# Kernel tuning notes

Hardware: AMD Instinct MI355X
Metric: run time of the kernel (lower is better)

Reference implementation:

```python
import jax, jax.numpy as jnp
import numpy as np

TEMPERATURE = 0.5


def setup_inputs() -> dict:
    key = jax.random.key(0)
    k1, k2 = jax.random.split(key)
    emb = jax.random.normal(k1, (16384, 128), dtype=jnp.float32)
    emb = emb / jnp.linalg.norm(emb, axis=1, keepdims=True)  # L2-normalized, per docstring
    labels = jax.random.randint(k2, (16384,), 0, 64, dtype=jnp.int64)
    return {"embeddings": emb, "partition_labels": labels}


def reference(embeddings, partition_labels):
    n = embeddings.shape[0]
    # [N, N] similarity matrix, scaled by temperature
    sim = jnp.matmul(embeddings, embeddings.T) / TEMPERATURE
    exp_sim = jnp.exp(sim)
    eye = jnp.eye(n, dtype=bool)
    pos_mask = (partition_labels[None, :] == partition_labels[:, None]) & ~eye
    # numerator: sum of exp over positives; denominator: sum over all k != i
    pos_sum = jnp.sum(jnp.where(pos_mask, exp_sim, 0.0), axis=1)
    all_sum = jnp.sum(jnp.where(~eye, exp_sim, 0.0), axis=1)
    valid = jnp.any(pos_mask, axis=1)
    loss_i = -(jnp.log(pos_sum) - jnp.log(all_sum))
    n_valid = jnp.sum(valid)
    total = jnp.sum(jnp.where(valid, loss_i, 0.0))
    return jnp.where(n_valid > 0, total / n_valid, 0.0)
```

## Files before the change

kernel.cpp:

```cpp
#include <hip/hip_runtime.h>

#define N_EMB 16384
#define DIM 128
#define NLAB 64
#define NSPLIT 8
#define NCT (N_EMB / NSPLIT / 128)
#define NT (N_EMB / 128)

typedef __bf16 bf16x8 __attribute__((ext_vector_type(8)));
typedef float f32x4 __attribute__((ext_vector_type(4)));
typedef unsigned short us8 __attribute__((ext_vector_type(8)));
typedef unsigned short us;
typedef unsigned int u32;

#define SCALE 2.8853900817779268f
#define LN2 0.6931471805599453f

__device__ inline float fexp2(float x) {
#if __has_builtin(__builtin_amdgcn_exp2f)
  return __builtin_amdgcn_exp2f(x);
#else
  return exp2f(x);
#endif
}
__device__ inline float flog2(float x) {
#if __has_builtin(__builtin_amdgcn_logf)
  return __builtin_amdgcn_logf(x);
#else
  return log2f(x);
#endif
}

__device__ inline us f2bf(float f) {
  u32 u = __float_as_uint(f);
  u += 0x7fffu + ((u >> 16) & 1u);
  return (us)(u >> 16);
}

__device__ inline void gll16(const us* g, us* l) {
  __builtin_amdgcn_global_load_lds(
      (const __attribute__((address_space(1))) u32*)g,
      (__attribute__((address_space(3))) u32*)l, 16, 0, 0);
}


__global__ void init_k(int* cntg, float* total) {
  if (threadIdx.x < NLAB) cntg[threadIdx.x] = 0;
  if (threadIdx.x == 0) *total = 0.f;
}

__global__ __launch_bounds__(256) void preconv(const float* __restrict__ emb,
                                               const int* __restrict__ labels,
                                               us* __restrict__ eraw,
                                               us* __restrict__ escal,
                                               int* __restrict__ cntg) {
  __shared__ int h[NLAB];
  const int tid = threadIdx.x;
  if (tid < NLAB) h[tid] = 0;
  __syncthreads();
  if (tid < 128) atomicAdd(&h[labels[blockIdx.x * 128 + tid]], 1);
  const size_t base = (size_t)blockIdx.x * 2048;
#pragma unroll
  for (int i = 0; i < 8; ++i) {
    int g = i * 256 + tid;
    int col16 = g & 15;
    int quad = (g >> 4) & 3;
    int ks = (g >> 6) & 3;
    int tc = g >> 8;
    const float* p = emb + ((size_t)blockIdx.x * 128 + tc * 16 + col16) * DIM +
                     ks * 32 + quad * 8;
    float4 a = *reinterpret_cast<const float4*>(p);
    float4 b = *reinterpret_cast<const float4*>(p + 4);
    us8 r, sc;
    r[0] = f2bf(a.x); r[1] = f2bf(a.y); r[2] = f2bf(a.z); r[3] = f2bf(a.w);
    r[4] = f2bf(b.x); r[5] = f2bf(b.y); r[6] = f2bf(b.z); r[7] = f2bf(b.w);
    sc[0] = f2bf(a.x * SCALE); sc[1] = f2bf(a.y * SCALE);
    sc[2] = f2bf(a.z * SCALE); sc[3] = f2bf(a.w * SCALE);
    sc[4] = f2bf(b.x * SCALE); sc[5] = f2bf(b.y * SCALE);
    sc[6] = f2bf(b.z * SCALE); sc[7] = f2bf(b.w * SCALE);
    *reinterpret_cast<us8*>(eraw + (base + g) * 8) = r;
    *reinterpret_cast<us8*>(escal + (base + g) * 8) = sc;
  }
  __syncthreads();
  if (tid < NLAB && h[tid] > 0) atomicAdd(&cntg[tid], h[tid]);
}

__global__ void scan_k(const int* __restrict__ cntg, int* offp, int* cursor) {
  int tid = threadIdx.x;
  int v = cntg[tid];
  int acc = 0;
#pragma unroll
  for (int k = 0; k < NLAB; ++k) {
    int ck = __shfl(v, k, 64);
    if (k < tid) acc += ck;
  }
  offp[tid] = acc;
  cursor[tid] = acc;
  if (tid == NLAB - 1) offp[NLAB] = acc + v;
}

__global__ void scatter_k(const int* __restrict__ labels, int* cursor,
                          int* perm) {
  __shared__ int lh[NLAB];
  __shared__ int base[NLAB];
  int tid = threadIdx.x;
  int i = blockIdx.x * 256 + tid;
  if (tid < NLAB) lh[tid] = 0;
  __syncthreads();
  int l = labels[i];
  int r = atomicAdd(&lh[l], 1);
  __syncthreads();
  if (tid < NLAB && lh[tid] > 0) base[tid] = atomicAdd(&cursor[tid], lh[tid]);
  __syncthreads();
  perm[base[l] + r] = i;
}

__global__ __launch_bounds__(128, 2) void cl_main(
    const us* __restrict__ eraw, const us* __restrict__ escal,
    float* __restrict__ ws_all) {
  __shared__ us lds[128 * DIM];

  const int tid = threadIdx.x;
  const int lane = tid & 63;
  const int w = tid >> 6;
  const int quad = lane >> 4;
  const int col16 = lane & 15;
  const int r0 = blockIdx.x * 128;
  const int cs = blockIdx.y;

  {
    const us* g = escal + (size_t)blockIdx.x * (128 * DIM);
#pragma unroll
    for (int i = 0; i < 16; ++i) {
      int chunk = i * 2 + w;
      gll16(g + chunk * 512 + lane * 8, lds + chunk * 512);
    }
  }
  __syncthreads();

  bf16x8 afrag[4][4];
#pragma unroll
  for (int tr = 0; tr < 4; ++tr)
#pragma unroll
    for (int ks = 0; ks < 4; ++ks)
      afrag[tr][ks] = *reinterpret_cast<const bf16x8*>(
          lds + ((w * 4 + tr) * 4 + ks) * 512 + lane * 8);

  float all_p[16];
#pragma unroll
  for (int t = 0; t < 16; ++t) all_p[t] = 0.f;

  for (int ct = 0; ct < NCT; ++ct) {
    const int ctg = cs * NCT + ct;
    __syncthreads();
    {
      const us* g = eraw + (size_t)ctg * (128 * DIM);
#pragma unroll
      for (int i = 0; i < 16; ++i) {
        int chunk = i * 2 + w;
        gll16(g + chunk * 512 + lane * 8, lds + chunk * 512);
      }
    }
    __syncthreads();

#pragma unroll
    for (int tc = 0; tc < 8; ++tc) {
      bf16x8 bf[4];
#pragma unroll
      for (int ks = 0; ks < 4; ++ks)
        bf[ks] = *reinterpret_cast<const bf16x8*>(lds + (tc * 4 + ks) * 512 +
                                                  lane * 8);
      const int c = ctg * 128 + tc * 16;
#pragma unroll
      for (int tr = 0; tr < 4; ++tr) {
        f32x4 acc = {0.f, 0.f, 0.f, 0.f};
#pragma unroll
        for (int ks = 0; ks < 4; ++ks)
          acc = __builtin_amdgcn_mfma_f32_16x16x32_bf16(afrag[tr][ks], bf[ks],
                                                        acc, 0, 0, 0);
        const bool diag = c == (r0 + w * 64 + tr * 16);
#pragma unroll
        for (int r = 0; r < 4; ++r) {
          float e = fexp2(acc[r]);
          if (diag && (quad * 4 + r) == col16) e = 0.f;
          all_p[tr * 4 + r] += e;
        }
      }
    }
  }

#pragma unroll
  for (int t = 0; t < 16; ++t) {
    float a = all_p[t];
#pragma unroll
    for (int m = 8; m >= 1; m >>= 1) a += __shfl_xor(a, m, 64);
    if (col16 == 0) {
      int row_g = r0 + w * 64 + (t >> 2) * 16 + quad * 4 + (t & 3);
      ws_all[cs * N_EMB + row_g] = a;
    }
  }
}

__global__ __launch_bounds__(256) void pos_loss(
    const us* __restrict__ eraw, const float* __restrict__ ws_all,
    const int* __restrict__ perm, const int* __restrict__ offp,
    const int* __restrict__ cntg, float* __restrict__ total) {
  const int l = blockIdx.x;
  const int c = cntg[l];
  if (c < 2) return;
  const int off = offp[l];
  const int strips = (c + 15) >> 4;
  const int tid = threadIdx.x;
  const int lane = tid & 63;
  const int w = tid >> 6;
  const int col16 = lane & 15;
  const int quad = lane >> 4;

  __shared__ float sred[4][16];

  bf16x8 zerov;
#pragma unroll
  for (int j = 0; j < 8; ++j) zerov[j] = (__bf16)0.f;

  for (int i = blockIdx.y; i < strips; i += gridDim.y) {
    bf16x8 af[4] = {zerov, zerov, zerov, zerov};
    int rowA = i * 16 + col16;
    if (rowA < c) {
      int rg = perm[off + rowA];
      const us* pA = eraw + ((size_t)(rg >> 7) * 2048 +
                             ((rg & 127) >> 4) * 256 + quad * 16 + (rg & 15)) *
                                8;
#pragma unroll
      for (int ks = 0; ks < 4; ++ks)
        af[ks] = *reinterpret_cast<const bf16x8*>(pA + ks * 512);
    }
    float sum[4] = {0.f, 0.f, 0.f, 0.f};
    for (int j = w; j < strips; j += 4) {
      bf16x8 bf[4] = {zerov, zerov, zerov, zerov};
      int rowB = j * 16 + col16;
      if (rowB < c) {
        int rg = perm[off + rowB];
        const us* pB =
            eraw + ((size_t)(rg >> 7) * 2048 + ((rg & 127) >> 4) * 256 +
                    quad * 16 + (rg & 15)) *
                       8;
#pragma unroll
        for (int ks = 0; ks < 4; ++ks)
          bf[ks] = *reinterpret_cast<const bf16x8*>(pB + ks * 512);
      }
      f32x4 acc = {0.f, 0.f, 0.f, 0.f};
#pragma unroll
      for (int ks = 0; ks < 4; ++ks)
        acc = __builtin_amdgcn_mfma_f32_16x16x32_bf16(af[ks], bf[ks], acc, 0,
                                                      0, 0);
      const float gm = (rowB < c) ? 1.f : 0.f;
#pragma unroll
      for (int r = 0; r < 4; ++r) {
        float e = fexp2(acc[r] * SCALE);
        if (i == j && (quad * 4 + r) == col16) e = 0.f;
        sum[r] = fmaf(e, gm, sum[r]);
      }
    }
#pragma unroll
    for (int r = 0; r < 4; ++r) {
      float s = sum[r];
#pragma unroll
      for (int m = 8; m >= 1; m >>= 1) s += __shfl_xor(s, m, 64);
      if (col16 == 0) sred[w][quad * 4 + r] = s;
    }
    __syncthreads();
    if (tid < 16) {
      int row = i * 16 + tid;
      float t = 0.f;
      if (row < c) {
        float p = sred[0][tid] + sred[1][tid] + sred[2][tid] + sred[3][tid];
        int rg = perm[off + row];
        float a = 0.f;
#pragma unroll
        for (int k = 0; k < NSPLIT; ++k) a += ws_all[k * N_EMB + rg];
        t = flog2(a) - flog2(p);
      }
#pragma unroll
      for (int m = 8; m >= 1; m >>= 1) t += __shfl_xor(t, m, 64);
      if (tid == 0) atomicAdd(total, t);
    }
    __syncthreads();
  }
}

__global__ void final_k(const float* __restrict__ total,
                        const int* __restrict__ cntg,
                        float* __restrict__ out) {
  int tid = threadIdx.x;
  int c = (tid < NLAB && cntg[tid] > 1) ? cntg[tid] : 0;
#pragma unroll
  for (int m = 32; m >= 1; m >>= 1) c += __shfl_xor(c, m, 64);
  if (tid == 0) out[0] = (c > 0) ? (*total) * LN2 / (float)c : 0.f;
}

extern "C" void kernel_launch(void* const* d_in, const int* in_sizes, int n_in,
                              void* d_out, int out_size, void* d_ws,
                              size_t ws_size, hipStream_t stream) {
  const float* emb = (const float*)d_in[0];
  const int* labels = (const int*)d_in[1];

  char* w = (char*)d_ws;
  us* eraw = (us*)w;         w += (size_t)N_EMB * DIM * 2;
  us* escal = (us*)w;        w += (size_t)N_EMB * DIM * 2;
  float* ws_all = (float*)w; w += (size_t)NSPLIT * N_EMB * 4;
  int* perm = (int*)w;       w += (size_t)N_EMB * 4;
  int* offp = (int*)w;       w += (NLAB + 1) * 4;
  int* cntg = (int*)w;       w += NLAB * 4;
  int* cursor = (int*)w;     w += NLAB * 4;
  float* total = (float*)w;

  init_k<<<1, 64, 0, stream>>>(cntg, total);
  preconv<<<NT, 256, 0, stream>>>(emb, labels, eraw, escal, cntg);
  scan_k<<<1, 64, 0, stream>>>(cntg, offp, cursor);
  scatter_k<<<N_EMB / 256, 256, 0, stream>>>(labels, cursor, perm);
  cl_main<<<dim3(NT, NSPLIT), 128, 0, stream>>>(eraw, escal, ws_all);
  pos_loss<<<dim3(NLAB, 20), 256, 0, stream>>>(eraw, ws_all, perm, offp, cntg,
                                               total);
  final_k<<<1, 64, 0, stream>>>(total, cntg, (float*)d_out);
}
```

Baseline: 167.7 us.

## Pre-gather label-sorted, 16-padded bf16 embeddings for coalesced positive-pair loads

Measured after the change: 166.2 us. About the same (-0.9%).

```diff
diff --git a/kernel.cpp b/kernel.cpp
--- a/kernel.cpp
+++ b/kernel.cpp
@@ -6,6 +6,8 @@
 #define NSPLIT 8
 #define NCT (N_EMB / NSPLIT / 128)
 #define NT (N_EMB / 128)
+#define NP 17408
+#define NTP (NP / 128)
 
 typedef __bf16 bf16x8 __attribute__((ext_vector_type(8)));
 typedef float f32x4 __attribute__((ext_vector_type(4)));
@@ -44,9 +46,11 @@
 }
 
 
-__global__ void init_k(int* cntg, float* total) {
-  if (threadIdx.x < NLAB) cntg[threadIdx.x] = 0;
-  if (threadIdx.x == 0) *total = 0.f;
+__global__ void init_k(int* perm_p, int* cntg, float* total) {
+  int i = blockIdx.x * 256 + threadIdx.x;
+  if (i < NP) perm_p[i] = -1;
+  if (blockIdx.x == 0 && threadIdx.x < NLAB) cntg[threadIdx.x] = 0;
+  if (blockIdx.x == 0 && threadIdx.x == 0) *total = 0.f;
 }
 
 __global__ __launch_bounds__(256) void preconv(const float* __restrict__ emb,
@@ -87,20 +91,19 @@
 
 __global__ void scan_k(const int* __restrict__ cntg, int* offp, int* cursor) {
   int tid = threadIdx.x;
-  int v = cntg[tid];
+  int pad = (cntg[tid] + 15) & ~15;
   int acc = 0;
 #pragma unroll
   for (int k = 0; k < NLAB; ++k) {
-    int ck = __shfl(v, k, 64);
+    int ck = __shfl(pad, k, 64);
     if (k < tid) acc += ck;
   }
   offp[tid] = acc;
   cursor[tid] = acc;
-  if (tid == NLAB - 1) offp[NLAB] = acc + v;
 }
 
 __global__ void scatter_k(const int* __restrict__ labels, int* cursor,
-                          int* perm) {
+                          int* perm_p) {
   __shared__ int lh[NLAB];
   __shared__ int base[NLAB];
   int tid = threadIdx.x;
@@ -112,7 +115,33 @@
   __syncthreads();
   if (tid < NLAB && lh[tid] > 0) base[tid] = atomicAdd(&cursor[tid], lh[tid]);
   __syncthreads();
-  perm[base[l] + r] = i;
+  perm_p[base[l] + r] = i;
+}
+
+__global__ __launch_bounds__(256) void esort_k(const float* __restrict__ emb,
+                                               const int* __restrict__ perm_p,
+                                               us* __restrict__ esort) {
+  const int tid = threadIdx.x;
+  const size_t base = (size_t)blockIdx.x * 2048;
+#pragma unroll
+  for (int i = 0; i < 8; ++i) {
+    int g = i * 256 + tid;
+    int col16 = g & 15;
+    int quad = (g >> 4) & 3;
+    int ks = (g >> 6) & 3;
+    int tc = g >> 8;
+    int slot = blockIdx.x * 128 + tc * 16 + col16;
+    int rg = perm_p[slot];
+    us8 r = {0, 0, 0, 0, 0, 0, 0, 0};
+    if (rg >= 0) {
+      const float* p = emb + (size_t)rg * DIM + ks * 32 + quad * 8;
+      float4 a = *reinterpret_cast<const float4*>(p);
+      float4 b = *reinterpret_cast<const float4*>(p + 4);
+      r[0] = f2bf(a.x); r[1] = f2bf(a.y); r[2] = f2bf(a.z); r[3] = f2bf(a.w);
+      r[4] = f2bf(b.x); r[5] = f2bf(b.y); r[6] = f2bf(b.z); r[7] = f2bf(b.w);
+    }
+    *reinterpret_cast<us8*>(esort + (base + g) * 8) = r;
+  }
 }
 
 __global__ __launch_bounds__(128, 2) void cl_main(
@@ -202,8 +231,8 @@
 }
 
 __global__ __launch_bounds__(256) void pos_loss(
-    const us* __restrict__ eraw, const float* __restrict__ ws_all,
-    const int* __restrict__ perm, const int* __restrict__ offp,
+    const us* __restrict__ esort, const float* __restrict__ ws_all,
+    const int* __restrict__ perm_p, const int* __restrict__ offp,
     const int* __restrict__ cntg, float* __restrict__ total) {
   const int l = blockIdx.x;
   const int c = cntg[l];
@@ -218,42 +247,29 @@
 
   __shared__ float sred[4][16];
 
-  bf16x8 zerov;
-#pragma unroll
-  for (int j = 0; j < 8; ++j) zerov[j] = (__bf16)0.f;
-
   for (int i = blockIdx.y; i < strips; i += gridDim.y) {
-    bf16x8 af[4] = {zerov, zerov, zerov, zerov};
-    int rowA = i * 16 + col16;
-    if (rowA < c) {
-      int rg = perm[off + rowA];
-      const us* pA = eraw + ((size_t)(rg >> 7) * 2048 +
-                             ((rg & 127) >> 4) * 256 + quad * 16 + (rg & 15)) *
-                                8;
-#pragma unroll
-      for (int ks = 0; ks < 4; ++ks)
-        af[ks] = *reinterpret_cast<const bf16x8*>(pA + ks * 512);
-    }
+    const int sA = off + i * 16;
+    const us* baseA = esort + ((size_t)(sA >> 7) * 2048 + ((sA & 127) >> 4) * 256) * 8;
+    bf16x8 af[4];
+#pragma unroll
+    for (int ks = 0; ks < 4; ++ks)
+      af[ks] = *reinterpret_cast<const bf16x8*>(baseA + (ks * 64 + lane) * 8);
+
     float sum[4] = {0.f, 0.f, 0.f, 0.f};
     for (int j = w; j < strips; j += 4) {
-      bf16x8 bf[4] = {zerov, zerov, zerov, zerov};
-      int rowB = j * 16 + col16;
-      if (rowB < c) {
-        int rg = perm[off + rowB];
-        const us* pB =
-            eraw + ((size_t)(rg >> 7) * 2048 + ((rg & 127) >> 4) * 256 +
-                    quad * 16 + (rg & 15)) *
-                       8;
-#pragma unroll
-        for (int ks = 0; ks < 4; ++ks)
-          bf[ks] = *reinterpret_cast<const bf16x8*>(pB + ks * 512);
-      }
+      const int sB = off + j * 16;
+      const us* baseB =
+          esort + ((size_t)(sB >> 7) * 2048 + ((sB & 127) >> 4) * 256) * 8;
+      bf16x8 bf[4];
+#pragma unroll
+      for (int ks = 0; ks < 4; ++ks)
+        bf[ks] = *reinterpret_cast<const bf16x8*>(baseB + (ks * 64 + lane) * 8);
       f32x4 acc = {0.f, 0.f, 0.f, 0.f};
 #pragma unroll
       for (int ks = 0; ks < 4; ++ks)
         acc = __builtin_amdgcn_mfma_f32_16x16x32_bf16(af[ks], bf[ks], acc, 0,
                                                       0, 0);
-      const float gm = (rowB < c) ? 1.f : 0.f;
+      const float gm = (j * 16 + col16 < c) ? 1.f : 0.f;
 #pragma unroll
       for (int r = 0; r < 4; ++r) {
         float e = fexp2(acc[r] * SCALE);
@@ -274,7 +290,7 @@
       float t = 0.f;
       if (row < c) {
         float p = sred[0][tid] + sred[1][tid] + sred[2][tid] + sred[3][tid];
-        int rg = perm[off + row];
+        int rg = perm_p[off + row];
         float a = 0.f;
 #pragma unroll
         for (int k = 0; k < NSPLIT; ++k) a += ws_all[k * N_EMB + rg];
@@ -307,19 +323,21 @@
   char* w = (char*)d_ws;
   us* eraw = (us*)w;         w += (size_t)N_EMB * DIM * 2;
   us* escal = (us*)w;        w += (size_t)N_EMB * DIM * 2;
+  us* esort = (us*)w;        w += (size_t)NP * DIM * 2;
   float* ws_all = (float*)w; w += (size_t)NSPLIT * N_EMB * 4;
-  int* perm = (int*)w;       w += (size_t)N_EMB * 4;
-  int* offp = (int*)w;       w += (NLAB + 1) * 4;
+  int* perm_p = (int*)w;     w += NP * 4;
+  int* offp = (int*)w;       w += NLAB * 4;
   int* cntg = (int*)w;       w += NLAB * 4;
   int* cursor = (int*)w;     w += NLAB * 4;
   float* total = (float*)w;
 
-  init_k<<<1, 64, 0, stream>>>(cntg, total);
+  init_k<<<(NP + 255) / 256, 256, 0, stream>>>(perm_p, cntg, total);
   preconv<<<NT, 256, 0, stream>>>(emb, labels, eraw, escal, cntg);
   scan_k<<<1, 64, 0, stream>>>(cntg, offp, cursor);
-  scatter_k<<<N_EMB / 256, 256, 0, stream>>>(labels, cursor, perm);
+  scatter_k<<<N_EMB / 256, 256, 0, stream>>>(labels, cursor, perm_p);
+  esort_k<<<NTP, 256, 0, stream>>>(emb, perm_p, esort);
   cl_main<<<dim3(NT, NSPLIT), 128, 0, stream>>>(eraw, escal, ws_all);
-  pos_loss<<<dim3(NLAB, 20), 256, 0, stream>>>(eraw, ws_all, perm, offp, cntg,
-                                               total);
+  pos_loss<<<dim3(NLAB, 20), 256, 0, stream>>>(esort, ws_all, perm_p, offp,
+                                               cntg, total);
   final_k<<<1, 64, 0, stream>>>(total, cntg, (float*)d_out);
 }
```
